# Kernel tuning notes

Measured on AMD Instinct MI355X. Metric: run time of the kernel, lower is better.

## Reference

```python
import jax, jax.numpy as jnp
import numpy as np

# SLAYER neuron / simulation parameters (from network.yaml)
THETA = 10.0      # spike threshold
TAU_SR = 10.0     # SRM (psp) kernel time constant
TAU_REF = 1.0     # refractory kernel time constant
SCALE_REF = 2.0   # refractory scale (kernel = -scaleRef*theta*alpha(t))
TS = 1.0          # simulation step (ms)
TK = 100          # FIR truncation length for the psp kernel (tauSr=10 -> fully decayed)

B, NIN, NHID, NOUT, T = 32, 2312, 512, 10, 350

# discrete refractory kernel ref[n] = C_REF * n * D_REF**n  (alpha shape)
D_REF = float(np.exp(-TS / TAU_REF))
C_REF = float(-SCALE_REF * THETA * np.e * TS / TAU_REF)


def srm_kernel():
    # eps(t) = (t/tauSr) * exp(1 - t/tauSr), peak value 1 at t = tauSr
    t = jnp.arange(TK, dtype=jnp.float32) * TS
    return (t / TAU_SR) * jnp.exp(1.0 - t / TAU_SR)


def psp(x):
    """Causal FIR filter along time. x: [B, C, T] -> [B, C, T]."""
    b, c, t = x.shape
    k = srm_kernel()[::-1].reshape(1, 1, TK)  # lax.conv correlates, so flip
    xp = jnp.pad(x.reshape(b * c, 1, t), ((0, 0), (0, 0), (TK - 1, 0)))
    y = jax.lax.conv_general_dilated(xp, k, (1,), 'VALID')
    return y.reshape(b, c, t)


def dense(W, x):
    # 1x1 conv over channels, applied at every time step
    return jnp.einsum('oi,bit->bot', W, x)


@jax.custom_vjp
def spike_fn(u):
    return (u >= THETA).astype(u.dtype)

def _spike_fwd(u):
    return spike_fn(u), u

def _spike_bwd(u, g):
    # SLAYER surrogate gradient: rho(u) = scaleRho * exp(-|u - theta| / tauRho)
    return (g * jnp.exp(-jnp.abs(u - THETA) / 1.0),)

spike_fn.defvjp(_spike_fwd, _spike_bwd)


def spike_layer(u_in):
    """Threshold-and-refractory spike dynamics via a 2-state IIR realization of
    the alpha refractory kernel. u_in: [B, C, T] -> spikes [B, C, T]."""
    uT = jnp.moveaxis(u_in, -1, 0)  # [T, B, C]
    zero = jnp.zeros(uT.shape[1:], uT.dtype)

    def step(carry, u_t):
        a, b = carry  # a = conv(spikes, D^n), b = conv(spikes, n*D^n)
        u = u_t + C_REF * b          # membrane = psp drive + refractory
        s = spike_fn(u)
        a_new = D_REF * a + s
        b_new = D_REF * b + D_REF * a
        return (a_new, b_new), s

    _, sT = jax.lax.scan(step, (zero, zero), uT)
    return jnp.moveaxis(sT, 0, -1)


def setup_inputs() -> dict:
    key = jax.random.key(0)
    k1, k2, k3 = jax.random.split(key, 3)
    spikeInput = (jax.random.uniform(k1, (B, NIN, T)) < 0.05).astype(jnp.float32)
    W1 = jax.random.normal(k2, (NHID, NIN), dtype=jnp.float32) * 0.05
    W2 = jax.random.normal(k3, (NOUT, NHID), dtype=jnp.float32) * 0.05
    return {"spikeInput": spikeInput, "W1": W1, "W2": W2}


def reference(spikeInput, W1, W2):
    s1 = spike_layer(dense(W1, psp(spikeInput)))
    s2 = spike_layer(dense(W2, psp(s1)))
    return s2
```

## Files before the change

### kernel.cpp

```cpp
#include <hip/hip_runtime.h>
#include <stdint.h>

#define B_SZ   32
#define NIN    2312
#define NHID   512
#define NOUT   10
#define T_SZ   350
#define NW32   73
#define NW64   8
#define NHALF  256
#define NROW   2313

#define DS_D   0.9048374180359595
#define CS_D   0.2718281828459045
#define D100_D 4.5399929762484854e-05
#define DREF_F 0.36787944117144233f
#define CREF_F -54.36563656918091f

#define NPF 14

__global__ __launch_bounds__(384) void k12(const float* __restrict__ x,
                                           const float* __restrict__ W1,
                                           uint32_t* __restrict__ bits1,
                                           float* __restrict__ W1s) {
    const int bid = blockIdx.x;
    const int tid = threadIdx.x;
    if (bid < NW32 * B_SZ) {
        const int w = bid % NW32;
        const int b = bid / NW32;
        if (tid < 175) {
            const int t2 = tid * 2;
            uint32_t bitsA = 0, bitsB = 0;
            const float* p = x + ((size_t)(b * NIN + (w << 5))) * T_SZ + t2;
#pragma unroll
            for (int j = 0; j < 32; ++j) {
                int i = (w << 5) + j;
                if (i < NIN) {
                    float2 v = *(const float2*)(p + (size_t)j * T_SZ);
                    if (v.x > 0.5f) bitsA |= (1u << j);
                    if (v.y > 0.5f) bitsB |= (1u << j);
                }
            }
            bits1[(size_t)(b * T_SZ + t2) * NW32 + w] = bitsA;
            bits1[(size_t)(b * T_SZ + t2 + 1) * NW32 + w] = bitsB;
        }
    } else if (bid < NW32 * B_SZ + NW32 * 16) {
        __shared__ float tile[32][33];
        const int bb = bid - NW32 * B_SZ;
        const int i0 = (bb % NW32) * 32, o0 = (bb / NW32) * 32;
        const int tx = tid & 31, ty = tid >> 5;
#pragma unroll
        for (int r = 0; r < 3; ++r) {
            int row = ty + 12 * r;
            if (row < 32) {
                int o = o0 + row, i = i0 + tx;
                if (i < NIN) tile[row][tx] = W1[(size_t)o * NIN + i];
            }
        }
        __syncthreads();
#pragma unroll
        for (int r = 0; r < 3; ++r) {
            int row = ty + 12 * r;
            if (row < 32) {
                int i = i0 + row, o = o0 + tx;
                if (i < NIN)
                    W1s[((size_t)(o >> 8) * NROW + i) * NHALF + (o & 255)] = tile[tx][row];
            }
        }
    } else {
        if (tid < NHALF) {
            W1s[((size_t)0 * NROW + NIN) * NHALF + tid] = 0.0f;
            W1s[((size_t)1 * NROW + NIN) * NHALF + tid] = 0.0f;
        }
    }
}

__global__ __launch_bounds__(256) void k3_dense1(const uint32_t* __restrict__ bits1,
                                                 const float* __restrict__ W1s,
                                                 float* __restrict__ z1ct) {
    __shared__ uint32_t words[128];
    __shared__ uint16_t pfx[80];
    __shared__ uint16_t idxbuf[NIN + 16];
    __shared__ float red[3][NHALF];
    __shared__ float fin[NHALF];

    const int bt = blockIdx.x;
    const int h = blockIdx.y;
    const int tid = threadIdx.x;
    const int wv = tid >> 6, lane = tid & 63;

    if (tid < 128) words[tid] = (tid < NW32) ? bits1[(size_t)bt * NW32 + tid] : 0u;
    __syncthreads();

    if (wv == 0) {
        uint32_t w0 = words[lane];
        uint32_t w1 = words[lane + 64];
        int p0 = __popc(w0), p1 = __popc(w1);
        int s0 = p0, s1 = p1;
#pragma unroll
        for (int off = 1; off < 64; off <<= 1) {
            int u0 = __shfl_up(s0, off);
            int u1 = __shfl_up(s1, off);
            if (lane >= off) { s0 += u0; s1 += u1; }
        }
        int tot0 = __shfl(s0, 63);
        pfx[lane] = (uint16_t)(s0 - p0);
        if (lane < 9) pfx[lane + 64] = (uint16_t)(tot0 + s1 - p1);
        if (lane == 8) pfx[73] = (uint16_t)(tot0 + s1);
    }
    __syncthreads();

    const int ntot = pfx[73];
    const int npad = (ntot + 15) & ~15;
    if (tid < NW32) {
        uint32_t m = words[tid];
        int p = pfx[tid];
        while (m) {
            int j = __builtin_ctz(m);
            m &= m - 1;
            idxbuf[p++] = (uint16_t)((tid << 5) + j);
        }
    }
    if (tid >= 240) {
        int k = tid - 240;
        if (ntot + k < npad) idxbuf[ntot + k] = (uint16_t)NIN;
    }
    __syncthreads();

    const float* Wh = W1s + (size_t)h * NROW * NHALF;
    float4 acc = make_float4(0.f, 0.f, 0.f, 0.f);
    for (int r = wv; r < npad; r += 16) {
        int i0 = idxbuf[r], i1 = idxbuf[r + 4], i2 = idxbuf[r + 8], i3 = idxbuf[r + 12];
        float4 v0 = ((const float4*)(Wh + (size_t)i0 * NHALF))[lane];
        float4 v1 = ((const float4*)(Wh + (size_t)i1 * NHALF))[lane];
        float4 v2 = ((const float4*)(Wh + (size_t)i2 * NHALF))[lane];
        float4 v3 = ((const float4*)(Wh + (size_t)i3 * NHALF))[lane];
        acc.x += v0.x; acc.y += v0.y; acc.z += v0.z; acc.w += v0.w;
        acc.x += v1.x; acc.y += v1.y; acc.z += v1.z; acc.w += v1.w;
        acc.x += v2.x; acc.y += v2.y; acc.z += v2.z; acc.w += v2.w;
        acc.x += v3.x; acc.y += v3.y; acc.z += v3.z; acc.w += v3.w;
    }
    if (wv > 0) ((float4*)red[wv - 1])[lane] = acc;
    __syncthreads();
    if (wv == 0) {
        float4 a1 = ((float4*)red[0])[lane];
        float4 a2 = ((float4*)red[1])[lane];
        float4 a3 = ((float4*)red[2])[lane];
        acc.x = ((acc.x + a1.x) + a2.x) + a3.x;
        acc.y = ((acc.y + a1.y) + a2.y) + a3.y;
        acc.z = ((acc.z + a1.z) + a2.z) + a3.z;
        acc.w = ((acc.w + a1.w) + a2.w) + a3.w;
        ((float4*)fin)[lane] = acc;
    }
    __syncthreads();
    const int och = (h << 8) + tid;
    const int oc = och >> 6, l6 = och & 63;
    const int b = bt / T_SZ, t = bt - b * T_SZ;
    z1ct[((size_t)(b * NW64 + oc) * T_SZ + t) * 64 + l6] = fin[tid];
}

__global__ __launch_bounds__(64) void k4_fir_scan1(const float* __restrict__ z1ct,
                                                   uint64_t* __restrict__ s1bits) {
    const int lane = threadIdx.x;
    const int bc = blockIdx.x;
    const float* base = z1ct + (size_t)bc * T_SZ * 64 + lane;
    uint64_t* outp = s1bits + (size_t)bc * T_SZ;
    double A = 0.0, Bs = 0.0, A2 = 0.0, Bs2 = 0.0;
    float ra = 0.0f, rb = 0.0f;
    const double TAIL = D100_D * CS_D;
    float xb[NPF], xdb[NPF];
#pragma unroll
    for (int i = 0; i < NPF; ++i) {
        xb[i] = base[(size_t)i * 64];
        xdb[i] = 0.0f;
    }
    for (int t0 = 0; t0 < T_SZ; t0 += NPF) {
#pragma unroll
        for (int i = 0; i < NPF; ++i) {
            const int t = t0 + i;
            float x = xb[i], xd = xdb[i];
            const int tn = t + NPF;
            xb[i] = (tn < T_SZ) ? base[(size_t)tn * 64] : 0.0f;
            const int td = tn - 100;
            xdb[i] = (td >= 0) ? base[(size_t)td * 64] : 0.0f;
            Bs = DS_D * Bs + DS_D * A;
            A = DS_D * A + (double)x;
            Bs2 = DS_D * Bs2 + DS_D * A2;
            A2 = DS_D * A2 + (double)xd;
            double y = CS_D * Bs - TAIL * (Bs2 + 100.0 * A2);
            float u = (float)y + CREF_F * rb;
            float s = (u >= 10.0f) ? 1.0f : 0.0f;
            float ran = DREF_F * ra + s;
            float rbn = DREF_F * rb + DREF_F * ra;
            ra = ran; rb = rbn;
            uint64_t mball = __ballot(s != 0.0f);
            if (lane == 0) outp[t] = mball;
        }
    }
}

__global__ __launch_bounds__(256) void k5_dense2(const uint64_t* __restrict__ s1bits,
                                                 const float* __restrict__ W2,
                                                 float* __restrict__ z2t) {
    __shared__ float W2s[NHID * NOUT];
    for (int k = threadIdx.x; k < NHID * NOUT; k += 256) {
        int c = k / NOUT, o = k - c * NOUT;
        W2s[k] = W2[(size_t)o * NHID + c];
    }
    __syncthreads();
    int idx = blockIdx.x * 256 + threadIdx.x;
    if (idx >= T_SZ * B_SZ * NOUT) return;
    int t = idx / (B_SZ * NOUT);
    int bo = idx - t * (B_SZ * NOUT);
    int b = bo / NOUT;
    int o = bo - b * NOUT;
    float acc = 0.f;
    const uint64_t* bp = s1bits + (size_t)b * NW64 * T_SZ + t;
#pragma unroll
    for (int wv = 0; wv < NW64; ++wv) {
        uint64_t m = bp[(size_t)wv * T_SZ];
        while (m) {
            int j = __builtin_ctzll(m);
            m &= m - 1;
            acc += W2s[((wv << 6) + j) * NOUT + o];
        }
    }
    z2t[idx] = acc;
}

__global__ __launch_bounds__(64) void k6_fir_scan2(const float* __restrict__ z2t,
                                                   float* __restrict__ out) {
    const int bo = blockIdx.x * 64 + threadIdx.x;
    const float* base = z2t + bo;
    double A = 0.0, Bs = 0.0, A2 = 0.0, Bs2 = 0.0;
    float ra = 0.0f, rb = 0.0f;
    const double TAIL = D100_D * CS_D;
    float* op = out + (size_t)bo * T_SZ;
    float xb[NPF], xdb[NPF];
#pragma unroll
    for (int i = 0; i < NPF; ++i) {
        xb[i] = base[(size_t)i * (B_SZ * NOUT)];
        xdb[i] = 0.0f;
    }
    for (int t0 = 0; t0 < T_SZ; t0 += NPF) {
#pragma unroll
        for (int i = 0; i < NPF; ++i) {
            const int t = t0 + i;
            float x = xb[i], xd = xdb[i];
            const int tn = t + NPF;
            xb[i] = (tn < T_SZ) ? base[(size_t)tn * (B_SZ * NOUT)] : 0.0f;
            const int td = tn - 100;
            xdb[i] = (td >= 0) ? base[(size_t)td * (B_SZ * NOUT)] : 0.0f;
            Bs = DS_D * Bs + DS_D * A;
            A = DS_D * A + (double)x;
            Bs2 = DS_D * Bs2 + DS_D * A2;
            A2 = DS_D * A2 + (double)xd;
            double y = CS_D * Bs - TAIL * (Bs2 + 100.0 * A2);
            float u = (float)y + CREF_F * rb;
            float s = (u >= 10.0f) ? 1.0f : 0.0f;
            float ran = DREF_F * ra + s;
            float rbn = DREF_F * rb + DREF_F * ra;
            ra = ran; rb = rbn;
            op[t] = s;
        }
    }
}

extern "C" void kernel_launch(void* const* d_in, const int* in_sizes, int n_in,
                              void* d_out, int out_size, void* d_ws, size_t ws_size,
                              hipStream_t stream) {
    const float* spikeInput = (const float*)d_in[0];
    const float* W1 = (const float*)d_in[1];
    const float* W2 = (const float*)d_in[2];
    float* out = (float*)d_out;

    char* ws = (char*)d_ws;
    float* W1s = (float*)(ws + 0);
    uint32_t* bits1 = (uint32_t*)(ws + 4737024);
    float* z1ct = (float*)(ws + 8007424);
    uint64_t* s1bits = (uint64_t*)(ws + 30945024);
    float* z2t = (float*)(ws + 4737024);

    k12<<<NW32 * B_SZ + NW32 * 16 + 1, 384, 0, stream>>>(spikeInput, W1, bits1, W1s);
    k3_dense1<<<dim3(B_SZ * T_SZ, 2), 256, 0, stream>>>(bits1, W1s, z1ct);
    k4_fir_scan1<<<B_SZ * NW64, 64, 0, stream>>>(z1ct, s1bits);
    k5_dense2<<<(T_SZ * B_SZ * NOUT + 255) / 256, 256, 0, stream>>>(s1bits, W2, z2t);
    k6_fir_scan2<<<(B_SZ * NOUT) / 64, 64, 0, stream>>>(z2t, out);
}
```

Measured before the change: 357.1 us.

## Split FIR/refractory time scans into overlapping chunks with warm-up

Both scan kernels now split the 350-step time axis into 7 chunks of 50 steps, each handled by its own block. Each block restarts from zero state 100 steps before its chunk; this is exact for the 100-tap FIR, and the refractory kernel has decayed to a negligible level over that span. The aim is to turn a long serial, latency-bound recurrence into many independent shorter ones, at the cost of redundant warm-up steps. The dense2 output is also re-laid out as [group][t][64] so the second scan reads coalesced 64-wide rows.

```diff
diff --git a/kernel.cpp b/kernel.cpp
--- a/kernel.cpp
+++ b/kernel.cpp
@@ -17,7 +17,9 @@
 #define DREF_F 0.36787944117144233f
 #define CREF_F -54.36563656918091f
 
-#define NPF 14
+#define NCHUNK 7
+#define CLEN   50
+#define NPF    10
 
 __global__ __launch_bounds__(384) void k12(const float* __restrict__ x,
                                            const float* __restrict__ W1,
@@ -162,7 +164,11 @@
 __global__ __launch_bounds__(64) void k4_fir_scan1(const float* __restrict__ z1ct,
                                                    uint64_t* __restrict__ s1bits) {
     const int lane = threadIdx.x;
-    const int bc = blockIdx.x;
+    const int bc = blockIdx.x / NCHUNK;
+    const int ck = blockIdx.x % NCHUNK;
+    const int tstart = ck * CLEN;
+    const int tend = tstart + CLEN;
+    const int t0 = (tstart >= 100) ? tstart - 100 : 0;
     const float* base = z1ct + (size_t)bc * T_SZ * 64 + lane;
     uint64_t* outp = s1bits + (size_t)bc * T_SZ;
     double A = 0.0, Bs = 0.0, A2 = 0.0, Bs2 = 0.0;
@@ -171,13 +177,15 @@
     float xb[NPF], xdb[NPF];
 #pragma unroll
     for (int i = 0; i < NPF; ++i) {
-        xb[i] = base[(size_t)i * 64];
-        xdb[i] = 0.0f;
-    }
-    for (int t0 = 0; t0 < T_SZ; t0 += NPF) {
+        int t = t0 + i;
+        xb[i] = base[(size_t)t * 64];
+        int td = t - 100;
+        xdb[i] = (td >= 0) ? base[(size_t)td * 64] : 0.0f;
+    }
+    for (int tb = t0; tb < tend; tb += NPF) {
 #pragma unroll
         for (int i = 0; i < NPF; ++i) {
-            const int t = t0 + i;
+            const int t = tb + i;
             float x = xb[i], xd = xdb[i];
             const int tn = t + NPF;
             xb[i] = (tn < T_SZ) ? base[(size_t)tn * 64] : 0.0f;
@@ -194,14 +202,14 @@
             float rbn = DREF_F * rb + DREF_F * ra;
             ra = ran; rb = rbn;
             uint64_t mball = __ballot(s != 0.0f);
-            if (lane == 0) outp[t] = mball;
+            if (t >= tstart && lane == 0) outp[t] = mball;
         }
     }
 }
 
 __global__ __launch_bounds__(256) void k5_dense2(const uint64_t* __restrict__ s1bits,
                                                  const float* __restrict__ W2,
-                                                 float* __restrict__ z2t) {
+                                                 float* __restrict__ z2ct) {
     __shared__ float W2s[NHID * NOUT];
     for (int k = threadIdx.x; k < NHID * NOUT; k += 256) {
         int c = k / NOUT, o = k - c * NOUT;
@@ -225,32 +233,40 @@
             acc += W2s[((wv << 6) + j) * NOUT + o];
         }
     }
-    z2t[idx] = acc;
-}
-
-__global__ __launch_bounds__(64) void k6_fir_scan2(const float* __restrict__ z2t,
+    z2ct[((size_t)(bo >> 6) * T_SZ + t) * 64 + (bo & 63)] = acc;
+}
+
+__global__ __launch_bounds__(64) void k6_fir_scan2(const float* __restrict__ z2ct,
                                                    float* __restrict__ out) {
-    const int bo = blockIdx.x * 64 + threadIdx.x;
-    const float* base = z2t + bo;
+    const int lane = threadIdx.x;
+    const int g = blockIdx.x / NCHUNK;
+    const int ck = blockIdx.x % NCHUNK;
+    const int tstart = ck * CLEN;
+    const int tend = tstart + CLEN;
+    const int t0 = (tstart >= 100) ? tstart - 100 : 0;
+    const int bo = (g << 6) + lane;
+    const float* base = z2ct + (size_t)g * T_SZ * 64 + lane;
+    float* op = out + (size_t)bo * T_SZ;
     double A = 0.0, Bs = 0.0, A2 = 0.0, Bs2 = 0.0;
     float ra = 0.0f, rb = 0.0f;
     const double TAIL = D100_D * CS_D;
-    float* op = out + (size_t)bo * T_SZ;
     float xb[NPF], xdb[NPF];
 #pragma unroll
     for (int i = 0; i < NPF; ++i) {
-        xb[i] = base[(size_t)i * (B_SZ * NOUT)];
-        xdb[i] = 0.0f;
-    }
-    for (int t0 = 0; t0 < T_SZ; t0 += NPF) {
+        int t = t0 + i;
+        xb[i] = base[(size_t)t * 64];
+        int td = t - 100;
+        xdb[i] = (td >= 0) ? base[(size_t)td * 64] : 0.0f;
+    }
+    for (int tb = t0; tb < tend; tb += NPF) {
 #pragma unroll
         for (int i = 0; i < NPF; ++i) {
-            const int t = t0 + i;
+            const int t = tb + i;
             float x = xb[i], xd = xdb[i];
             const int tn = t + NPF;
-            xb[i] = (tn < T_SZ) ? base[(size_t)tn * (B_SZ * NOUT)] : 0.0f;
+            xb[i] = (tn < T_SZ) ? base[(size_t)tn * 64] : 0.0f;
             const int td = tn - 100;
-            xdb[i] = (td >= 0) ? base[(size_t)td * (B_SZ * NOUT)] : 0.0f;
+            xdb[i] = (td >= 0) ? base[(size_t)td * 64] : 0.0f;
             Bs = DS_D * Bs + DS_D * A;
             A = DS_D * A + (double)x;
             Bs2 = DS_D * Bs2 + DS_D * A2;
@@ -261,7 +277,7 @@
             float ran = DREF_F * ra + s;
             float rbn = DREF_F * rb + DREF_F * ra;
             ra = ran; rb = rbn;
-            op[t] = s;
+            if (t >= tstart) op[t] = s;
         }
     }
 }
@@ -279,11 +295,11 @@
     uint32_t* bits1 = (uint32_t*)(ws + 4737024);
     float* z1ct = (float*)(ws + 8007424);
     uint64_t* s1bits = (uint64_t*)(ws + 30945024);
-    float* z2t = (float*)(ws + 4737024);
+    float* z2ct = (float*)(ws + 4737024);
 
     k12<<<NW32 * B_SZ + NW32 * 16 + 1, 384, 0, stream>>>(spikeInput, W1, bits1, W1s);
     k3_dense1<<<dim3(B_SZ * T_SZ, 2), 256, 0, stream>>>(bits1, W1s, z1ct);
-    k4_fir_scan1<<<B_SZ * NW64, 64, 0, stream>>>(z1ct, s1bits);
-    k5_dense2<<<(T_SZ * B_SZ * NOUT + 255) / 256, 256, 0, stream>>>(s1bits, W2, z2t);
-    k6_fir_scan2<<<(B_SZ * NOUT) / 64, 64, 0, stream>>>(z2t, out);
-}
+    k4_fir_scan1<<<B_SZ * NW64 * NCHUNK, 64, 0, stream>>>(z1ct, s1bits);
+    k5_dense2<<<(T_SZ * B_SZ * NOUT + 255) / 256, 256, 0, stream>>>(s1bits, W2, z2ct);
+    k6_fir_scan2<<<5 * NCHUNK, 64, 0, stream>>>(z2ct, out);
+}
```

Result: faster. 335.7 us (-6.0%).
